# Kernel tuning notes

Measured on AMD Instinct MI355X. Metric: run time of the kernel, lower is better.

The kernel has to match this reference:

```python
import jax, jax.numpy as jnp
import numpy as np

B, T = 16, 2048
OBS_DIM, ACT_DIM, HIDDEN = 64, 16, 512


def setup_inputs() -> dict:
    key = jax.random.key(0)
    ks = jax.random.split(key, 6)
    n = lambda k, shape, scale: (jax.random.normal(k, shape, dtype=jnp.float32) * scale)
    return {
        "obs": n(ks[0], (B, T, OBS_DIM), 1.0),
        "act": n(ks[1], (B, T, ACT_DIM), 1.0),
        "W_e": n(ks[2], (HIDDEN, OBS_DIM + ACT_DIM), 0.05),   # embed Linear weight
        "b_e": jnp.zeros((HIDDEN,), jnp.float32),             # embed Linear bias
        "a_raw": n(ks[3], (HIDDEN,), 0.5),                    # diagonal decay (pre-tanh)
        "W_B": n(ks[4], (HIDDEN, HIDDEN), 0.02),              # B Linear weight (no bias)
        "W_out": n(ks[5], (OBS_DIM, HIDDEN), 0.04),           # out Linear weight
        "b_out": jnp.zeros((OBS_DIM,), jnp.float32),          # out Linear bias
    }


def reference(obs, act, W_e, b_e, a_raw, W_B, W_out, b_out):
    # x: [B, T, obs+act]
    x = jnp.concatenate([obs, act], axis=-1)
    # embed: Linear + ReLU, batched over all timesteps -> u: [B, T, H]
    u = jax.nn.relu(jnp.einsum('btd,hd->bth', x, W_e) + b_e)
    # B projection batched over all t (the per-step matmul in the torch loop)
    v = jnp.einsum('bth,gh->btg', u, W_B)  # [B, T, H]
    a = jnp.tanh(a_raw)  # [H]
    # Diagonal linear recurrence s_t = a * s_{t-1} + v_t, s_0 starting from zeros,
    # realized as a parallel (log-depth) associative scan over (decay, input) pairs.
    A = jnp.broadcast_to(a, v.shape)
    def combine(c1, c2):
        a1, b1 = c1
        a2, b2 = c2
        return (a1 * a2, a2 * b1 + b2)
    _, s = jax.lax.associative_scan(combine, (A, v), axis=1)  # s: [B, T, H]
    # out projection per step -> preds: [B, T, obs_dim]
    return jnp.einsum('bth,oh->bto', s, W_out) + b_out
```

## Files before the change

kernel.cpp:

```cpp
#include <hip/hip_runtime.h>
#include <hip/hip_bf16.h>

#define B_    16
#define T_    2048
#define H_    512
#define BT_   32768
#define DIN   80
#define DPAD  96
#define L_    64
#define C_    32
#define O_    64
#define NCHUNK (BT_ / L_)

typedef __attribute__((ext_vector_type(8))) short short8;
typedef __attribute__((ext_vector_type(4))) float f32x4;
typedef __attribute__((ext_vector_type(4))) float float4v;

__device__ __forceinline__ float bf2f(unsigned short u) {
  union { unsigned int i; float f; } x; x.i = ((unsigned int)u) << 16; return x.f;
}
__device__ __forceinline__ unsigned short f2bf(float f) {
  union { float f; unsigned int i; } x; x.f = f;
  unsigned int r = x.i + 0x7fffu + ((x.i >> 16) & 1u);
  return (unsigned short)(r >> 16);
}

template<int BM, int BN, int BK, int RELU, int BIAS, int OUTBF, int CE, int XS>
__global__ __launch_bounds__(256) void gemm_bt(
    const unsigned short* __restrict__ A, const unsigned short* __restrict__ Bt,
    const float* __restrict__ bias, void* __restrict__ Cv,
    int M, int N, int K,
    const float* __restrict__ powa,
    float* __restrict__ e)
{
  constexpr int WAVES_N = 2;
  constexpr int WM = BM / 2, WN = BN / WAVES_N;
  constexpr int FM = WM / 16, FN = WN / 16;
  constexpr int A_BYTES = BM * BK * 2;
  constexpr int TOT = A_BYTES + BN * BK * 2;
  constexpr int ROUNDS = TOT / 4096;
  __shared__ __align__(16) unsigned char ldsb[2 * TOT];

  const int tid  = threadIdx.x;
  const int lane = tid & 63;
  const int wid  = tid >> 6;
  const int wr   = wid >> 1, wc = wid & 1;

  int bid = (int)blockIdx.x;
  if (XS) {
    const int cpx = (int)gridDim.x >> 3;
    bid = (bid & 7) * cpx + (bid >> 3);
  }
  const int nb   = N / BN;
  const int mt   = bid / nb, nt = bid % nb;
  const int row0 = mt * BM, col0 = nt * BN;

  auto stage = [&](int k0, int buf) {
    #pragma unroll
    for (int r = 0; r < ROUNDS; ++r) {
      const int o = r * 4096 + tid * 16;
      const unsigned short* gsrc;
      if (o < A_BYTES) {
        const int idx = o >> 1;
        const int row = idx / BK, kk = idx % BK;
        gsrc = A + (size_t)(row0 + row) * K + (k0 + kk);
      } else {
        const int idx = (o - A_BYTES) >> 1;
        const int row = idx / BK, kk = idx % BK;
        gsrc = Bt + (size_t)(col0 + row) * K + (k0 + kk);
      }
      __builtin_amdgcn_global_load_lds(
          (const __attribute__((address_space(1))) void*)gsrc,
          (__attribute__((address_space(3))) void*)(ldsb + buf * TOT + o),
          16, 0, 0);
    }
  };

  f32x4 acc[FM][FN];
  #pragma unroll
  for (int m = 0; m < FM; ++m)
    #pragma unroll
    for (int n = 0; n < FN; ++n) acc[m][n] = f32x4{0.f, 0.f, 0.f, 0.f};

  const int NT = K / BK;
  stage(0, 0);
  __syncthreads();
  int cur = 0;
  for (int t = 0; t < NT; ++t) {
    if (t + 1 < NT) stage((t + 1) * BK, cur ^ 1);

    const unsigned short* base = (const unsigned short*)(ldsb + cur * TOT);
    const unsigned short* pA = base + (wr * WM + (lane & 15)) * BK + ((lane >> 4) * 8);
    const unsigned short* pB = base + (A_BYTES / 2) + (wc * WN + (lane & 15)) * BK + ((lane >> 4) * 8);
    short8 af[FM], bfr[FN];
    #pragma unroll
    for (int m = 0; m < FM; ++m) af[m] = *(const short8*)(pA + m * 16 * BK);
    #pragma unroll
    for (int n = 0; n < FN; ++n) bfr[n] = *(const short8*)(pB + n * 16 * BK);
    #pragma unroll
    for (int m = 0; m < FM; ++m)
      #pragma unroll
      for (int n = 0; n < FN; ++n)
        acc[m][n] = __builtin_amdgcn_mfma_f32_16x16x32_bf16(af[m], bfr[n], acc[m][n], 0, 0, 0);

    __syncthreads();
    cur ^= 1;
  }

  const int cl = lane & 15, rg = (lane >> 4) * 4;
  #pragma unroll
  for (int m = 0; m < FM; ++m) {
    #pragma unroll
    for (int n = 0; n < FN; ++n) {
      #pragma unroll
      for (int e2 = 0; e2 < 4; ++e2) {
        const int gr = row0 + wr * WM + m * 16 + rg + e2;
        const int gc = col0 + wc * WN + n * 16 + cl;
        float v = acc[m][n][e2];
        if (BIAS) v += bias[gc];
        if (RELU) v = fmaxf(v, 0.f);
        if (OUTBF) ((unsigned short*)Cv)[(size_t)gr * N + gc] = f2bf(v);
        else       ((float*)Cv)[(size_t)gr * N + gc] = v;
      }
    }
  }

  if (CE) {
    const int chunk = (row0 + wr * WM) >> 6;
    #pragma unroll
    for (int n = 0; n < FN; ++n) {
      const int h = col0 + wc * WN + n * 16 + cl;
      const float a16 = powa[15 * H_ + h];
      float ep = 0.f;
      #pragma unroll
      for (int e2 = 0; e2 < 4; ++e2) {
        const int k = 15 - rg - e2;
        const float wk = (k == 0) ? 1.f : powa[(size_t)(k - 1) * H_ + h];
        float hsum = acc[0][n][e2];
        hsum = fmaf(hsum, a16, acc[1][n][e2]);
        hsum = fmaf(hsum, a16, acc[2][n][e2]);
        hsum = fmaf(hsum, a16, acc[3][n][e2]);
        ep = fmaf(wk, hsum, ep);
      }
      ep += __shfl_xor(ep, 16);
      ep += __shfl_xor(ep, 32);
      if ((lane >> 4) == 0)
        e[(size_t)chunk * H_ + h] = ep;
    }
  }
}

__global__ __launch_bounds__(256) void prep_x(
    const float* __restrict__ obs, const float* __restrict__ act,
    unsigned short* __restrict__ xb)
{
  const int idx = blockIdx.x * 256 + threadIdx.x;
  const int g = idx % 12, n = idx / 12;
  float f[8];
  if (g < 8) {
    const float4v f0 = ((const float4v*)obs)[(size_t)n * 16 + g * 2];
    const float4v f1 = ((const float4v*)obs)[(size_t)n * 16 + g * 2 + 1];
    f[0]=f0[0]; f[1]=f0[1]; f[2]=f0[2]; f[3]=f0[3];
    f[4]=f1[0]; f[5]=f1[1]; f[6]=f1[2]; f[7]=f1[3];
  } else if (g < 10) {
    const float4v f0 = ((const float4v*)act)[(size_t)n * 4 + (g - 8) * 2];
    const float4v f1 = ((const float4v*)act)[(size_t)n * 4 + (g - 8) * 2 + 1];
    f[0]=f0[0]; f[1]=f0[1]; f[2]=f0[2]; f[3]=f0[3];
    f[4]=f1[0]; f[5]=f1[1]; f[6]=f1[2]; f[7]=f1[3];
  } else {
    #pragma unroll
    for (int i = 0; i < 8; ++i) f[i] = 0.f;
  }
  short8 o;
  #pragma unroll
  for (int i = 0; i < 8; ++i) o[i] = (short)f2bf(f[i]);
  *(short8*)(xb + (size_t)idx * 8) = o;
}

#define WE_N  (H_ * DPAD)
#define WB_N  (H_ * H_)
#define WO_N  (O_ * H_)
#define PREP_TOT (WE_N + WB_N + WO_N + H_)

__global__ __launch_bounds__(256) void prep_w(
    const float* __restrict__ W_e, const float* __restrict__ W_B,
    const float* __restrict__ W_out, const float* __restrict__ a_raw,
    unsigned short* __restrict__ Web, unsigned short* __restrict__ WBb,
    unsigned short* __restrict__ Woutb, float* __restrict__ aarr,
    float* __restrict__ powa)
{
  const int idx = blockIdx.x * 256 + threadIdx.x;
  if (idx < WE_N) {
    const int h = idx / DPAD, d = idx % DPAD;
    Web[idx] = f2bf(d < DIN ? W_e[h * DIN + d] : 0.f);
  } else if (idx < WE_N + WB_N) {
    const int j = idx - WE_N;
    WBb[j] = f2bf(W_B[j]);
  } else if (idx < WE_N + WB_N + WO_N) {
    const int j = idx - (WE_N + WB_N);
    Woutb[j] = f2bf(W_out[j]);
  } else if (idx < PREP_TOT) {
    const int h = idx - (WE_N + WB_N + WO_N);
    const float a = tanhf(a_raw[h]);
    aarr[h] = a;
    float p = a;
    #pragma unroll
    for (int i = 0; i < 16; ++i) { powa[i * H_ + h] = p; p *= a; }
  }
}

__global__ __launch_bounds__(256) void carry_scan(
    const float* __restrict__ e, float* __restrict__ P,
    const float* __restrict__ aarr)
{
  const int idx = blockIdx.x * 256 + threadIdx.x;
  const int b = idx >> 9, h = idx & (H_ - 1);
  const float a = aarr[h];
  float aL = a * a; aL *= aL; aL *= aL; aL *= aL; aL *= aL; aL *= aL;
  float S = 0.f;
  for (int c = 0; c < C_; ++c) {
    const size_t o = ((size_t)(b * C_ + c)) * H_ + h;
    P[o] = S;
    S = fmaf(aL, S, e[o]);
  }
}

__global__ __launch_bounds__(256) void scan_out(
    const unsigned int* __restrict__ v,
    const float* __restrict__ P,
    const float* __restrict__ aarr,
    const unsigned short* __restrict__ Wo,
    const float* __restrict__ b_out,
    float* __restrict__ y)
{
  __shared__ __align__(16) unsigned char sbytes[64 * 1024];
  const int blk = blockIdx.x;
  const int tid = threadIdx.x;
  const int lane = tid & 63, w = tid >> 6;
  const int row_base = blk * L_;

  {
    const int h0 = tid * 2;
    const float a0 = aarr[h0], a1 = aarr[h0 + 1];
    float s0 = P[(size_t)blk * H_ + h0];
    float s1 = P[(size_t)blk * H_ + h0 + 1];
    const unsigned int* vp = v + (size_t)row_base * (H_ / 2) + tid;
    #pragma unroll 8
    for (int t = 0; t < L_; ++t) {
      const unsigned int pv = vp[(size_t)t * (H_ / 2)];
      s0 = fmaf(a0, s0, bf2f((unsigned short)(pv & 0xffff)));
      s1 = fmaf(a1, s1, bf2f((unsigned short)(pv >> 16)));
      const int byte = t * 1024 + ((tid * 4) ^ ((t & 7) << 4));
      *(unsigned int*)(sbytes + byte) =
          (unsigned int)f2bf(s0) | ((unsigned int)f2bf(s1) << 16);
    }
  }
  __syncthreads();

  f32x4 acc[4];
  #pragma unroll
  for (int n = 0; n < 4; ++n) acc[n] = f32x4{0.f, 0.f, 0.f, 0.f};
  const int r = w * 16 + (lane & 15);
  const int kof = (lane >> 4) * 8;
  #pragma unroll 4
  for (int k0 = 0; k0 < H_; k0 += 32) {
    const int byte = r * 1024 + (((k0 + kof) * 2) ^ ((r & 7) << 4));
    const short8 af = *(const short8*)(sbytes + byte);
    #pragma unroll
    for (int n = 0; n < 4; ++n) {
      const short8 bf = *(const short8*)(Wo + (size_t)(n * 16 + (lane & 15)) * H_ + k0 + kof);
      acc[n] = __builtin_amdgcn_mfma_f32_16x16x32_bf16(af, bf, acc[n], 0, 0, 0);
    }
  }
  const int cl = lane & 15, rg = (lane >> 4) * 4;
  #pragma unroll
  for (int n = 0; n < 4; ++n) {
    #pragma unroll
    for (int e2 = 0; e2 < 4; ++e2) {
      const int gr = row_base + w * 16 + rg + e2;
      const int gc = n * 16 + cl;
      y[(size_t)gr * O_ + gc] = acc[n][e2] + b_out[gc];
    }
  }
}

extern "C" void kernel_launch(void* const* d_in, const int* in_sizes, int n_in,
                              void* d_out, int out_size, void* d_ws, size_t ws_size,
                              hipStream_t stream)
{
  const float* obs   = (const float*)d_in[0];
  const float* act   = (const float*)d_in[1];
  const float* W_e   = (const float*)d_in[2];
  const float* b_e   = (const float*)d_in[3];
  const float* a_raw = (const float*)d_in[4];
  const float* W_B   = (const float*)d_in[5];
  const float* W_out = (const float*)d_in[6];
  const float* b_out = (const float*)d_in[7];
  float* y = (float*)d_out;

  char* w = (char*)d_ws;
  auto carve = [&](size_t bytes) {
    char* p = w; w += (bytes + 255) & ~(size_t)255; return p;
  };
  unsigned short* xb    = (unsigned short*)carve((size_t)BT_ * DPAD * 2);
  unsigned short* Web   = (unsigned short*)carve((size_t)H_ * DPAD * 2);
  unsigned short* WBb   = (unsigned short*)carve((size_t)H_ * H_ * 2);
  unsigned short* Woutb = (unsigned short*)carve((size_t)O_ * H_ * 2);
  float*          aarr  = (float*)carve((size_t)H_ * 4);
  float*          powa  = (float*)carve((size_t)16 * H_ * 4);
  unsigned short* u     = (unsigned short*)carve((size_t)BT_ * H_ * 2);
  unsigned short* v     = (unsigned short*)carve((size_t)BT_ * H_ * 2);
  float*          e     = (float*)carve((size_t)NCHUNK * H_ * 4);
  float*          P     = (float*)carve((size_t)NCHUNK * H_ * 4);

  prep_x<<<BT_ * 12 / 256, 256, 0, stream>>>(obs, act, xb);
  prep_w<<<(PREP_TOT + 255) / 256, 256, 0, stream>>>(W_e, W_B, W_out, a_raw,
                                                     Web, WBb, Woutb, aarr, powa);
  gemm_bt<128, 128, 32, 1, 1, 1, 0, 1><<<(BT_ / 128) * (H_ / 128), 256, 0, stream>>>(
      xb, Web, b_e, u, BT_, H_, DPAD, nullptr, nullptr);
  gemm_bt<128, 128, 32, 0, 0, 1, 1, 1><<<(BT_ / 128) * (H_ / 128), 256, 0, stream>>>(
      u, WBb, nullptr, v, BT_, H_, H_, powa, e);
  carry_scan<<<(B_ * H_) / 256, 256, 0, stream>>>(e, P, aarr);
  scan_out<<<NCHUNK, 256, 0, stream>>>((const unsigned int*)v, P, aarr,
                                       Woutb, b_out, y);
}
```

Before: 79.28 us.

## Merge prep kernels, drop carry_scan, use full-width 128x512 GEMM tiles

The two prep kernels become a single launch, and the separate carry_scan kernel is removed: each scan_out block now recomputes its chunk's incoming carry by serially folding the preceding chunk sums. Both GEMMs switch to 512-thread blocks covering all 512 output columns (128x512 tiles, 8 waves), so each A tile is loaded once and B fragments are reused across four M fragments. This cuts the launch count from six to four and removes redundant A traffic. The cost is up to 31 redundant carry steps per scan block, a larger LDS and register footprint per GEMM block, and only 256 GEMM blocks.

```diff
diff --git a/kernel.cpp b/kernel.cpp
--- a/kernel.cpp
+++ b/kernel.cpp
@@ -25,40 +25,31 @@
   return (unsigned short)(r >> 16);
 }
 
-template<int BM, int BN, int BK, int RELU, int BIAS, int OUTBF, int CE, int XS>
-__global__ __launch_bounds__(256) void gemm_bt(
+template<int RELU, int BIAS, int CE>
+__global__ __launch_bounds__(512) void gemm_fn(
     const unsigned short* __restrict__ A, const unsigned short* __restrict__ Bt,
-    const float* __restrict__ bias, void* __restrict__ Cv,
-    int M, int N, int K,
+    const float* __restrict__ bias, unsigned short* __restrict__ Cb,
+    int K,
     const float* __restrict__ powa,
     float* __restrict__ e)
 {
-  constexpr int WAVES_N = 2;
-  constexpr int WM = BM / 2, WN = BN / WAVES_N;
-  constexpr int FM = WM / 16, FN = WN / 16;
+  constexpr int BM = 128, BN = 512, BK = 32;
   constexpr int A_BYTES = BM * BK * 2;
   constexpr int TOT = A_BYTES + BN * BK * 2;
-  constexpr int ROUNDS = TOT / 4096;
+  constexpr int ROUNDS = TOT / (512 * 16);
   __shared__ __align__(16) unsigned char ldsb[2 * TOT];
 
   const int tid  = threadIdx.x;
   const int lane = tid & 63;
   const int wid  = tid >> 6;
-  const int wr   = wid >> 1, wc = wid & 1;
-
-  int bid = (int)blockIdx.x;
-  if (XS) {
-    const int cpx = (int)gridDim.x >> 3;
-    bid = (bid & 7) * cpx + (bid >> 3);
-  }
-  const int nb   = N / BN;
-  const int mt   = bid / nb, nt = bid % nb;
-  const int row0 = mt * BM, col0 = nt * BN;
+  const int wr   = wid >> 2;
+  const int wc   = wid & 3;
+  const int row0 = (int)blockIdx.x * BM;
 
   auto stage = [&](int k0, int buf) {
     #pragma unroll
     for (int r = 0; r < ROUNDS; ++r) {
-      const int o = r * 4096 + tid * 16;
+      const int o = r * 8192 + tid * 16;
       const unsigned short* gsrc;
       if (o < A_BYTES) {
         const int idx = o >> 1;
@@ -67,7 +58,7 @@
       } else {
         const int idx = (o - A_BYTES) >> 1;
         const int row = idx / BK, kk = idx % BK;
-        gsrc = Bt + (size_t)(col0 + row) * K + (k0 + kk);
+        gsrc = Bt + (size_t)row * K + (k0 + kk);
       }
       __builtin_amdgcn_global_load_lds(
           (const __attribute__((address_space(1))) void*)gsrc,
@@ -76,11 +67,11 @@
     }
   };
 
-  f32x4 acc[FM][FN];
+  f32x4 acc[4][8];
   #pragma unroll
-  for (int m = 0; m < FM; ++m)
-    #pragma unroll
-    for (int n = 0; n < FN; ++n) acc[m][n] = f32x4{0.f, 0.f, 0.f, 0.f};
+  for (int m = 0; m < 4; ++m)
+    #pragma unroll
+    for (int n = 0; n < 8; ++n) acc[m][n] = f32x4{0.f, 0.f, 0.f, 0.f};
 
   const int NT = K / BK;
   stage(0, 0);
@@ -90,18 +81,18 @@
     if (t + 1 < NT) stage((t + 1) * BK, cur ^ 1);
 
     const unsigned short* base = (const unsigned short*)(ldsb + cur * TOT);
-    const unsigned short* pA = base + (wr * WM + (lane & 15)) * BK + ((lane >> 4) * 8);
-    const unsigned short* pB = base + (A_BYTES / 2) + (wc * WN + (lane & 15)) * BK + ((lane >> 4) * 8);
-    short8 af[FM], bfr[FN];
-    #pragma unroll
-    for (int m = 0; m < FM; ++m) af[m] = *(const short8*)(pA + m * 16 * BK);
-    #pragma unroll
-    for (int n = 0; n < FN; ++n) bfr[n] = *(const short8*)(pB + n * 16 * BK);
-    #pragma unroll
-    for (int m = 0; m < FM; ++m)
+    const unsigned short* pA = base + (wr * 64 + (lane & 15)) * BK + ((lane >> 4) * 8);
+    const unsigned short* pB = base + (A_BYTES / 2) + (wc * 128 + (lane & 15)) * BK + ((lane >> 4) * 8);
+    short8 af[4];
+    #pragma unroll
+    for (int m = 0; m < 4; ++m) af[m] = *(const short8*)(pA + m * 16 * BK);
+    #pragma unroll
+    for (int n = 0; n < 8; ++n) {
+      const short8 bfr = *(const short8*)(pB + n * 16 * BK);
       #pragma unroll
-      for (int n = 0; n < FN; ++n)
-        acc[m][n] = __builtin_amdgcn_mfma_f32_16x16x32_bf16(af[m], bfr[n], acc[m][n], 0, 0, 0);
+      for (int m = 0; m < 4; ++m)
+        acc[m][n] = __builtin_amdgcn_mfma_f32_16x16x32_bf16(af[m], bfr, acc[m][n], 0, 0, 0);
+    }
 
     __syncthreads();
     cur ^= 1;
@@ -109,27 +100,26 @@
 
   const int cl = lane & 15, rg = (lane >> 4) * 4;
   #pragma unroll
-  for (int m = 0; m < FM; ++m) {
-    #pragma unroll
-    for (int n = 0; n < FN; ++n) {
+  for (int m = 0; m < 4; ++m) {
+    #pragma unroll
+    for (int n = 0; n < 8; ++n) {
       #pragma unroll
       for (int e2 = 0; e2 < 4; ++e2) {
-        const int gr = row0 + wr * WM + m * 16 + rg + e2;
-        const int gc = col0 + wc * WN + n * 16 + cl;
+        const int gr = row0 + wr * 64 + m * 16 + rg + e2;
+        const int gc = wc * 128 + n * 16 + cl;
         float v = acc[m][n][e2];
         if (BIAS) v += bias[gc];
         if (RELU) v = fmaxf(v, 0.f);
-        if (OUTBF) ((unsigned short*)Cv)[(size_t)gr * N + gc] = f2bf(v);
-        else       ((float*)Cv)[(size_t)gr * N + gc] = v;
+        Cb[(size_t)gr * BN + gc] = f2bf(v);
       }
     }
   }
 
   if (CE) {
-    const int chunk = (row0 + wr * WM) >> 6;
-    #pragma unroll
-    for (int n = 0; n < FN; ++n) {
-      const int h = col0 + wc * WN + n * 16 + cl;
+    const int chunk = (row0 + wr * 64) >> 6;
+    #pragma unroll
+    for (int n = 0; n < 8; ++n) {
+      const int h = wc * 128 + n * 16 + cl;
       const float a16 = powa[15 * H_ + h];
       float ep = 0.f;
       #pragma unroll
@@ -150,46 +140,47 @@
   }
 }
 
-__global__ __launch_bounds__(256) void prep_x(
-    const float* __restrict__ obs, const float* __restrict__ act,
-    unsigned short* __restrict__ xb)
-{
-  const int idx = blockIdx.x * 256 + threadIdx.x;
-  const int g = idx % 12, n = idx / 12;
-  float f[8];
-  if (g < 8) {
-    const float4v f0 = ((const float4v*)obs)[(size_t)n * 16 + g * 2];
-    const float4v f1 = ((const float4v*)obs)[(size_t)n * 16 + g * 2 + 1];
-    f[0]=f0[0]; f[1]=f0[1]; f[2]=f0[2]; f[3]=f0[3];
-    f[4]=f1[0]; f[5]=f1[1]; f[6]=f1[2]; f[7]=f1[3];
-  } else if (g < 10) {
-    const float4v f0 = ((const float4v*)act)[(size_t)n * 4 + (g - 8) * 2];
-    const float4v f1 = ((const float4v*)act)[(size_t)n * 4 + (g - 8) * 2 + 1];
-    f[0]=f0[0]; f[1]=f0[1]; f[2]=f0[2]; f[3]=f0[3];
-    f[4]=f1[0]; f[5]=f1[1]; f[6]=f1[2]; f[7]=f1[3];
-  } else {
-    #pragma unroll
-    for (int i = 0; i < 8; ++i) f[i] = 0.f;
-  }
-  short8 o;
-  #pragma unroll
-  for (int i = 0; i < 8; ++i) o[i] = (short)f2bf(f[i]);
-  *(short8*)(xb + (size_t)idx * 8) = o;
-}
-
+#define PX_N  (BT_ * 12)
 #define WE_N  (H_ * DPAD)
 #define WB_N  (H_ * H_)
 #define WO_N  (O_ * H_)
-#define PREP_TOT (WE_N + WB_N + WO_N + H_)
-
-__global__ __launch_bounds__(256) void prep_w(
+#define PW_N  (WE_N + WB_N + WO_N + H_)
+#define PREP_THREADS (PX_N + PW_N)
+
+__global__ __launch_bounds__(256) void prep(
+    const float* __restrict__ obs, const float* __restrict__ act,
     const float* __restrict__ W_e, const float* __restrict__ W_B,
     const float* __restrict__ W_out, const float* __restrict__ a_raw,
+    unsigned short* __restrict__ xb,
     unsigned short* __restrict__ Web, unsigned short* __restrict__ WBb,
     unsigned short* __restrict__ Woutb, float* __restrict__ aarr,
     float* __restrict__ powa)
 {
-  const int idx = blockIdx.x * 256 + threadIdx.x;
+  const int gid = blockIdx.x * 256 + threadIdx.x;
+  if (gid < PX_N) {
+    const int g = gid % 12, n = gid / 12;
+    float f[8];
+    if (g < 8) {
+      const float4v f0 = ((const float4v*)obs)[(size_t)n * 16 + g * 2];
+      const float4v f1 = ((const float4v*)obs)[(size_t)n * 16 + g * 2 + 1];
+      f[0]=f0[0]; f[1]=f0[1]; f[2]=f0[2]; f[3]=f0[3];
+      f[4]=f1[0]; f[5]=f1[1]; f[6]=f1[2]; f[7]=f1[3];
+    } else if (g < 10) {
+      const float4v f0 = ((const float4v*)act)[(size_t)n * 4 + (g - 8) * 2];
+      const float4v f1 = ((const float4v*)act)[(size_t)n * 4 + (g - 8) * 2 + 1];
+      f[0]=f0[0]; f[1]=f0[1]; f[2]=f0[2]; f[3]=f0[3];
+      f[4]=f1[0]; f[5]=f1[1]; f[6]=f1[2]; f[7]=f1[3];
+    } else {
+      #pragma unroll
+      for (int i = 0; i < 8; ++i) f[i] = 0.f;
+    }
+    short8 o;
+    #pragma unroll
+    for (int i = 0; i < 8; ++i) o[i] = (short)f2bf(f[i]);
+    *(short8*)(xb + (size_t)gid * 8) = o;
+    return;
+  }
+  const int idx = gid - PX_N;
   if (idx < WE_N) {
     const int h = idx / DPAD, d = idx % DPAD;
     Web[idx] = f2bf(d < DIN ? W_e[h * DIN + d] : 0.f);
@@ -199,7 +190,7 @@
   } else if (idx < WE_N + WB_N + WO_N) {
     const int j = idx - (WE_N + WB_N);
     Woutb[j] = f2bf(W_out[j]);
-  } else if (idx < PREP_TOT) {
+  } else if (idx < PW_N) {
     const int h = idx - (WE_N + WB_N + WO_N);
     const float a = tanhf(a_raw[h]);
     aarr[h] = a;
@@ -209,25 +200,9 @@
   }
 }
 
-__global__ __launch_bounds__(256) void carry_scan(
-    const float* __restrict__ e, float* __restrict__ P,
-    const float* __restrict__ aarr)
-{
-  const int idx = blockIdx.x * 256 + threadIdx.x;
-  const int b = idx >> 9, h = idx & (H_ - 1);
-  const float a = aarr[h];
-  float aL = a * a; aL *= aL; aL *= aL; aL *= aL; aL *= aL; aL *= aL;
-  float S = 0.f;
-  for (int c = 0; c < C_; ++c) {
-    const size_t o = ((size_t)(b * C_ + c)) * H_ + h;
-    P[o] = S;
-    S = fmaf(aL, S, e[o]);
-  }
-}
-
 __global__ __launch_bounds__(256) void scan_out(
     const unsigned int* __restrict__ v,
-    const float* __restrict__ P,
+    const float* __restrict__ e,
     const float* __restrict__ aarr,
     const unsigned short* __restrict__ Wo,
     const float* __restrict__ b_out,
@@ -235,6 +210,7 @@
 {
   __shared__ __align__(16) unsigned char sbytes[64 * 1024];
   const int blk = blockIdx.x;
+  const int b = blk >> 5, c = blk & 31;
   const int tid = threadIdx.x;
   const int lane = tid & 63, w = tid >> 6;
   const int row_base = blk * L_;
@@ -242,8 +218,18 @@
   {
     const int h0 = tid * 2;
     const float a0 = aarr[h0], a1 = aarr[h0 + 1];
-    float s0 = P[(size_t)blk * H_ + h0];
-    float s1 = P[(size_t)blk * H_ + h0 + 1];
+    float aL0 = a0 * a0, aL1 = a1 * a1;
+    aL0 *= aL0; aL1 *= aL1;
+    aL0 *= aL0; aL1 *= aL1;
+    aL0 *= aL0; aL1 *= aL1;
+    aL0 *= aL0; aL1 *= aL1;
+    aL0 *= aL0; aL1 *= aL1;
+    float s0 = 0.f, s1 = 0.f;
+    for (int j = 0; j < c; ++j) {
+      const size_t o = ((size_t)(b * C_ + j)) * H_ + h0;
+      s0 = fmaf(aL0, s0, e[o]);
+      s1 = fmaf(aL1, s1, e[o + 1]);
+    }
     const unsigned int* vp = v + (size_t)row_base * (H_ / 2) + tid;
     #pragma unroll 8
     for (int t = 0; t < L_; ++t) {
@@ -311,16 +297,14 @@
   unsigned short* u     = (unsigned short*)carve((size_t)BT_ * H_ * 2);
   unsigned short* v     = (unsigned short*)carve((size_t)BT_ * H_ * 2);
   float*          e     = (float*)carve((size_t)NCHUNK * H_ * 4);
-  float*          P     = (float*)carve((size_t)NCHUNK * H_ * 4);
-
-  prep_x<<<BT_ * 12 / 256, 256, 0, stream>>>(obs, act, xb);
-  prep_w<<<(PREP_TOT + 255) / 256, 256, 0, stream>>>(W_e, W_B, W_out, a_raw,
-                                                     Web, WBb, Woutb, aarr, powa);
-  gemm_bt<128, 128, 32, 1, 1, 1, 0, 1><<<(BT_ / 128) * (H_ / 128), 256, 0, stream>>>(
-      xb, Web, b_e, u, BT_, H_, DPAD, nullptr, nullptr);
-  gemm_bt<128, 128, 32, 0, 0, 1, 1, 1><<<(BT_ / 128) * (H_ / 128), 256, 0, stream>>>(
-      u, WBb, nullptr, v, BT_, H_, H_, powa, e);
-  carry_scan<<<(B_ * H_) / 256, 256, 0, stream>>>(e, P, aarr);
-  scan_out<<<NCHUNK, 256, 0, stream>>>((const unsigned int*)v, P, aarr,
+
+  prep<<<PREP_THREADS / 256, 256, 0, stream>>>(obs, act, W_e, W_B, W_out,
+                                               a_raw, xb, Web, WBb, Woutb,
+                                               aarr, powa);
+  gemm_fn<1, 1, 0><<<BT_ / 128, 512, 0, stream>>>(
+      xb, Web, b_e, u, DPAD, nullptr, nullptr);
+  gemm_fn<0, 0, 1><<<BT_ / 128, 512, 0, stream>>>(
+      u, WBb, nullptr, v, H_, powa, e);
+  scan_out<<<NCHUNK, 256, 0, stream>>>((const unsigned int*)v, e, aarr,
                                        Woutb, b_out, y);
 }
```

Result: no change. 79.03 us (-0.3%).
